# Optimization experiments

Measured on AMD Instinct MI355X. Metric: run time of the kernel, lower is better.

The kernel has to match this reference:

```python
import jax, jax.numpy as jnp
import numpy as np

N, E, F_IN, H, C, ED, NODES = 25000, 100000, 16, 4, 280, 6, 6


def setup_inputs() -> dict:
    key = jax.random.key(0)
    ks = jax.random.split(key, 16)
    s = lambda k, sh: jax.random.normal(k, sh, dtype=jnp.float32) * 0.05
    return {
        "x": jax.random.normal(ks[0], (N, F_IN), dtype=jnp.float32),
        "edge_index": jax.random.randint(ks[1], (2, E), 0, N, dtype=jnp.int64),
        "edge_attr": jax.random.normal(ks[2], (E, ED), dtype=jnp.float32),
        # TransformerConv params (PyG): lin_query/key/value (bias), lin_edge (no bias), lin_skip (bias)
        "Wq": s(ks[3], (F_IN, H * C)), "bq": jnp.zeros((H * C,), jnp.float32),
        "Wk": s(ks[4], (F_IN, H * C)), "bk": jnp.zeros((H * C,), jnp.float32),
        "Wv": s(ks[5], (F_IN, H * C)), "bv": jnp.zeros((H * C,), jnp.float32),
        "We": s(ks[6], (ED, H * C)),
        "Wskip": s(ks[7], (F_IN, C)), "bskip": jnp.zeros((C,), jnp.float32),
        # MLP: 280 -> 64 -> 16 -> NODES, softmax
        "W1": s(ks[8], (280, 64)), "b1": jnp.zeros((64,), jnp.float32),
        "W2": s(ks[9], (64, 16)), "b2": jnp.zeros((16,), jnp.float32),
        "W3": s(ks[10], (16, NODES)), "b3": jnp.zeros((NODES,), jnp.float32),
    }


def reference(x, edge_index, edge_attr, Wq, bq, Wk, bk, Wv, bv, We, Wskip, bskip, W1, b1, W2, b2, W3, b3):
    n = x.shape[0]
    src, dst = edge_index[0], edge_index[1]  # message j -> i (PyG convention)
    q = (x @ Wq + bq).reshape(n, H, C)
    k = (x @ Wk + bk).reshape(n, H, C)
    v = (x @ Wv + bv).reshape(n, H, C)
    e = (edge_attr @ We).reshape(-1, H, C)  # [E,H,C]
    kj = k[src] + e                          # gather + edge features
    alpha = jnp.einsum('ehc,ehc->eh', q[dst], kj) / jnp.sqrt(jnp.float32(C))  # [E,H]
    # numerically stable segment softmax over destination nodes
    amax = jax.ops.segment_max(alpha, dst, num_segments=n)
    ex = jnp.exp(alpha - amax[dst])
    denom = jax.ops.segment_sum(ex, dst, num_segments=n)
    attn = ex / (denom[dst] + 1e-16)
    out = jax.ops.segment_sum(attn[..., None] * (v[src] + e), dst, num_segments=n)  # [N,H,C]
    out = out.mean(axis=1)                  # concat=False -> mean over heads
    out = out + x @ Wskip + bskip           # root/skip connection
    h = out.reshape(-1, 280)
    h = jax.nn.relu(h @ W1 + b1)
    h = jax.nn.relu(h @ W2 + b2)
    return jax.nn.softmax(h @ W3 + b3, axis=-1)
```

## Files before the change

### kernel.cpp

```cpp
#include <hip/hip_runtime.h>

#define N_NODES 25000
#define N_EDGES 100000
#define NPAD 25024
#define CH 280
#define HC 1120
#define CAP 32

typedef unsigned int uint;
typedef unsigned short ushort;
typedef __attribute__((ext_vector_type(8))) short short8;
typedef __attribute__((ext_vector_type(4))) float f32x4;

#define FAC_A 0
#define FAC_B 1024
#define FAC_C 1408
#define FAC_D 1472
#define FAC_F 1536
#define FAC_G 1560
#define FAC_TOTAL 1564

#define WC_K 128

#define PREP_FAC_END   25
#define PREP_WC_END    54
#define PREP_W2_END    55
#define PREP_FILL_END  446
#define PREP_TOTAL     544

__device__ __forceinline__ ushort f2bf(float f) {
  union { float f; uint u; } c; c.f = f;
  uint u = c.u + 0x7FFFu + ((c.u >> 16) & 1u);
  return (ushort)(u >> 16);
}

__global__ __launch_bounds__(256) void prep_kernel(
    const float* __restrict__ Wq, const float* __restrict__ Wk,
    const float* __restrict__ We, const float* __restrict__ bq,
    const float* __restrict__ bk, float* __restrict__ fac,
    const float* __restrict__ Wv, const float* __restrict__ bv,
    const float* __restrict__ Wskip, const float* __restrict__ bskip,
    const float* __restrict__ W1, const float* __restrict__ b1,
    ushort* __restrict__ Wct,
    const float* __restrict__ W2, ushort* __restrict__ W2tg,
    const int* __restrict__ ei, const float* __restrict__ ea,
    int* __restrict__ cursor, float* __restrict__ erec,
    const float* __restrict__ x, ushort* __restrict__ Vb) {
  int b = blockIdx.x;
  if (b < PREP_FAC_END) {
    int t4 = b * 256 + threadIdx.x;
    int q = t4 >> 2, li = t4 & 3;
    if (q >= FAC_TOTAL) return;
    const float *pa, *pb;
    if (q < FAC_B) {
      int h = q >> 8, f = (q >> 4) & 15, g = q & 15;
      pa = Wq + f * HC + h * CH; pb = Wk + g * HC + h * CH;
    } else if (q < FAC_C) {
      int u = q - FAC_B; int h = u / 96, v2 = u % 96, f = v2 / 6, j = v2 % 6;
      pa = Wq + f * HC + h * CH; pb = We + j * HC + h * CH;
    } else if (q < FAC_D) {
      int u = q - FAC_C; int h = u >> 4, f = u & 15;
      pa = Wq + f * HC + h * CH; pb = bk + h * CH;
    } else if (q < FAC_F) {
      int u = q - FAC_D; int h = u >> 4, g = u & 15;
      pa = Wk + g * HC + h * CH; pb = bq + h * CH;
    } else if (q < FAC_G) {
      int u = q - FAC_F; int h = u / 6, j = u % 6;
      pa = We + j * HC + h * CH; pb = bq + h * CH;
    } else {
      int h = q - FAC_G;
      pa = bq + h * CH; pb = bk + h * CH;
    }
    float acc = 0.f;
    int c0 = li * 70;
    for (int c = c0; c < c0 + 70; ++c) acc = fmaf(pa[c], pb[c], acc);
    acc += __shfl_xor(acc, 1);
    acc += __shfl_xor(acc, 2);
    if (li == 0) fac[q] = acc;
  } else if (b < PREP_WC_END) {
    int wid = threadIdx.x >> 6;
    int r = __builtin_amdgcn_readfirstlane((b - PREP_FAC_END) * 4 + wid);
    if (r >= 113) return;
    int k = threadIdx.x & 63;
    const float* w = nullptr;
    float scale = 1.f;
    bool zero = false;
    if (r < 96) {
      int h = r / 24, j = r % 24;
      if (j == 23) zero = true;
      else {
        if (j < 16) w = Wv + j * HC + h * CH;
        else if (j < 22) w = We + (j - 16) * HC + h * CH;
        else w = bv + h * CH;
        scale = 0.25f;
      }
    } else if (r < 112) {
      w = Wskip + (r - 96) * CH;
    } else {
      w = bskip;
    }
    if (zero) return;
    float acc = 0.f;
    for (int c = 0; c < CH; ++c) acc = fmaf(w[c], W1[c * 64 + k], acc);
    float v = acc * scale;
    if (r == 112) v += b1[k];
    Wct[k * WC_K + r] = f2bf(v);
  } else if (b < PREP_W2_END) {
    for (int t = threadIdx.x; t < 1024; t += 256) {
      int m2 = t >> 6, k = t & 63;
      W2tg[m2 * 64 + k] = f2bf(W2[(size_t)k * 16 + m2]);
    }
  } else if (b < PREP_FILL_END) {
    int e = (b - PREP_W2_END) * 256 + threadIdx.x;
    if (e >= N_EDGES) return;
    int src = ei[e];
    int dst = ei[N_EDGES + e];
    int pos = atomicAdd(&cursor[dst], 1);
    if (pos >= CAP) return;
    const float2* s2 = (const float2*)(ea + (size_t)e * 6);
    float2 e01 = s2[0], e23 = s2[1], e45 = s2[2];
    int4 w0;
    w0.x = src;
    w0.y = __float_as_int(e01.x); w0.z = __float_as_int(e01.y);
    w0.w = __float_as_int(e23.x);
    float4 w1 = make_float4(e23.y, e45.x, e45.y, 0.f);
    float* dstp = erec + ((size_t)dst * CAP + pos) * 8;
    *(int4*)dstp = w0;
    *(float4*)(dstp + 4) = w1;
  } else {
    int n = (b - PREP_FILL_END) * 256 + threadIdx.x;
    if (n >= N_NODES) return;
    const float4* x4 = (const float4*)(x + (size_t)n * 16);
    float xv[16];
#pragma unroll
    for (int i = 0; i < 4; ++i) {
      float4 q = x4[i];
      xv[4 * i] = q.x; xv[4 * i + 1] = q.y; xv[4 * i + 2] = q.z; xv[4 * i + 3] = q.w;
    }
    uint pk[8];
#pragma unroll
    for (int i = 0; i < 8; ++i)
      pk[i] = (uint)f2bf(xv[2 * i]) | ((uint)f2bf(xv[2 * i + 1]) << 16);
    int4* vp = (int4*)(Vb + (size_t)n * WC_K + 96);
    int4 s0, s1, s2, s3;
    s0.x = (int)pk[0]; s0.y = (int)pk[1]; s0.z = (int)pk[2]; s0.w = (int)pk[3];
    s1.x = (int)pk[4]; s1.y = (int)pk[5]; s1.z = (int)pk[6]; s1.w = (int)pk[7];
    s2.x = (int)0x3F80u; s2.y = 0; s2.z = 0; s2.w = 0;
    s3.x = 0; s3.y = 0; s3.z = 0; s3.w = 0;
    vp[0] = s0; vp[1] = s1; vp[2] = s2; vp[3] = s3;
  }
}

__global__ __launch_bounds__(256) void attn_kernel(
    const float* __restrict__ x, const float* __restrict__ fac,
    const float* __restrict__ erec, const int* __restrict__ cursor,
    ushort* __restrict__ Vb) {
  const float RS = 0.05976143046671968f;
  int h = blockIdx.y;
  int wid = threadIdx.x >> 6, lane = threadIdx.x & 63;
  int sub = lane >> 2, half = lane & 3;
  int n = (blockIdx.x * 4 + wid) * 16 + sub;
  if (n >= N_NODES) return;
  float xv[16];
  {
    const float4* x4 = (const float4*)(x + (size_t)n * 16);
#pragma unroll
    for (int i = 0; i < 4; ++i) {
      float4 q = x4[i];
      xv[4 * i] = q.x; xv[4 * i + 1] = q.y; xv[4 * i + 2] = q.z; xv[4 * i + 3] = q.w;
    }
  }
  const float* A  = fac + FAC_A + h * 256;
  const float* B  = fac + FAC_B + h * 96;
  const float* cf = fac + FAC_C + h * 16;
  const float* df = fac + FAC_D + h * 16;
  const float* ff = fac + FAC_F + h * 6;
  const float  gf = fac[FAC_G + h];
  float va[16];
#pragma unroll
  for (int g = 0; g < 16; ++g) {
    float a = df[g];
#pragma unroll
    for (int f = 0; f < 16; ++f) a = fmaf(xv[f], A[f * 16 + g], a);
    va[g] = a;
  }
  float ve[6];
#pragma unroll
  for (int j = 0; j < 6; ++j) {
    float a = ff[j];
#pragma unroll
    for (int f = 0; f < 16; ++f) a = fmaf(xv[f], B[f * 6 + j], a);
    ve[j] = a;
  }
  float v22 = gf;
#pragma unroll
  for (int f = 0; f < 16; ++f) v22 = fmaf(xv[f], cf[f], v22);

  int dg = cursor[n];
  if (dg > CAP) dg = CAP;
  float m = -1e30f, den = 0.f;
  float Sx[16];
  float Sa[6];
#pragma unroll
  for (int f = 0; f < 16; ++f) Sx[f] = 0.f;
#pragma unroll
  for (int j = 0; j < 6; ++j) Sa[j] = 0.f;
  for (int q2 = half; q2 < dg; q2 += 4) {
    const float* er = erec + ((size_t)n * CAP + q2) * 8;
    int4 ra = *(const int4*)er;
    float4 rb = *(const float4*)(er + 4);
    int s = ra.x;
    const float4* xs4 = (const float4*)(x + (size_t)s * 16);
    float4 a0 = xs4[0], a1 = xs4[1], a2 = xs4[2], a3 = xs4[3];
    float xs[16] = {a0.x, a0.y, a0.z, a0.w, a1.x, a1.y, a1.z, a1.w,
                    a2.x, a2.y, a2.z, a2.w, a3.x, a3.y, a3.z, a3.w};
    float eav[6] = {__int_as_float(ra.y), __int_as_float(ra.z),
                    __int_as_float(ra.w), rb.x, rb.y, rb.z};
    float alpha = v22;
#pragma unroll
    for (int f = 0; f < 16; ++f) alpha = fmaf(va[f], xs[f], alpha);
#pragma unroll
    for (int j = 0; j < 6; ++j) alpha = fmaf(ve[j], eav[j], alpha);
    alpha *= RS;
    float nm = fmaxf(m, alpha);
    float sc = __expf(m - nm);
    float w = __expf(alpha - nm);
    den = den * sc + w;
#pragma unroll
    for (int f = 0; f < 16; ++f) Sx[f] = fmaf(Sx[f], sc, w * xs[f]);
#pragma unroll
    for (int j = 0; j < 6; ++j) Sa[j] = fmaf(Sa[j], sc, w * eav[j]);
    m = nm;
  }
#pragma unroll
  for (int d = 1; d <= 2; d <<= 1) {
    float mo  = __shfl_xor(m, d);
    float dno = __shfl_xor(den, d);
    float mm = fmaxf(m, mo);
    float sa = __expf(m - mm);
    float sb = __expf(mo - mm);
    den = den * sa + dno * sb;
#pragma unroll
    for (int f = 0; f < 16; ++f) {
      float so = __shfl_xor(Sx[f], d);
      Sx[f] = Sx[f] * sa + so * sb;
    }
#pragma unroll
    for (int j = 0; j < 6; ++j) {
      float so = __shfl_xor(Sa[j], d);
      Sa[j] = Sa[j] * sa + so * sb;
    }
    m = mm;
  }
  if (half) return;
  float inv = 1.f / (den + 1e-16f);
  float outv[24];
#pragma unroll
  for (int f = 0; f < 16; ++f) outv[f] = Sx[f] * inv;
#pragma unroll
  for (int j = 0; j < 6; ++j) outv[16 + j] = Sa[j] * inv;
  outv[22] = den * inv;
  outv[23] = 0.f;
  uint pk[12];
#pragma unroll
  for (int i = 0; i < 12; ++i)
    pk[i] = (uint)f2bf(outv[2 * i]) | ((uint)f2bf(outv[2 * i + 1]) << 16);
  int4* vp = (int4*)(Vb + (size_t)n * WC_K + h * 24);
  int4 s0, s1, s2;
  s0.x = (int)pk[0]; s0.y = (int)pk[1]; s0.z = (int)pk[2]; s0.w = (int)pk[3];
  s1.x = (int)pk[4]; s1.y = (int)pk[5]; s1.z = (int)pk[6]; s1.w = (int)pk[7];
  s2.x = (int)pk[8]; s2.y = (int)pk[9]; s2.z = (int)pk[10]; s2.w = (int)pk[11];
  vp[0] = s0; vp[1] = s1; vp[2] = s2;
}

__global__ __launch_bounds__(256) void mlp_kernel(
    const ushort* __restrict__ Vb, const ushort* __restrict__ Wct,
    const ushort* __restrict__ W2tg, const float* __restrict__ b2,
    const float* __restrict__ W3, const float* __restrict__ b3,
    float* __restrict__ out) {
  __shared__ ushort Wcs[64 * 136];
  __shared__ ushort W2ts[16 * 72];
  __shared__ ushort h1b[64 * 72];
  __shared__ float  h2s[64 * 17];
  int tid = threadIdx.x;
  int wid = tid >> 6, lane = tid & 63;
  int col15 = lane & 15, quad = lane >> 4;
  {
    int row = tid >> 2, seg = tid & 3;
    const ushort* src = Wct + row * 128 + seg * 32;
    ushort* dst = Wcs + row * 136 + seg * 32;
#pragma unroll
    for (int i = 0; i < 4; ++i)
      *(int4*)(dst + i * 8) = *(const int4*)(src + i * 8);
  }
  if (tid < 128) {
    int row = tid >> 3, seg = tid & 7;
    *(int4*)(W2ts + row * 72 + seg * 8) = *(const int4*)(W2tg + row * 64 + seg * 8);
  }
  __syncthreads();
  int node = blockIdx.x * 64 + wid * 16 + col15;
  f32x4 acc[4];
#pragma unroll
  for (int T = 0; T < 4; ++T) acc[T] = (f32x4){0.f, 0.f, 0.f, 0.f};
#pragma unroll
  for (int kk = 0; kk < 4; ++kk) {
    int k0 = kk * 32;
    short8 a = *(const short8*)(Vb + (size_t)node * WC_K + k0 + quad * 8);
#pragma unroll
    for (int T = 0; T < 4; ++T) {
      short8 bfr = *(const short8*)(Wcs + (T * 16 + col15) * 136 + k0 + quad * 8);
      acc[T] = __builtin_amdgcn_mfma_f32_16x16x32_bf16(a, bfr, acc[T], 0, 0, 0);
    }
  }
#pragma unroll
  for (int T = 0; T < 4; ++T) {
#pragma unroll
    for (int r = 0; r < 4; ++r) {
      int nloc = wid * 16 + quad * 4 + r;
      int c = T * 16 + col15;
      h1b[nloc * 72 + c] = f2bf(fmaxf(acc[T][r], 0.f));
    }
  }
  __syncthreads();
  float b2v = b2[col15];
  f32x4 acc2 = (f32x4){0.f, 0.f, 0.f, 0.f};
#pragma unroll
  for (int kk = 0; kk < 2; ++kk) {
    int k0 = kk * 32;
    short8 a2 = *(const short8*)(h1b + (wid * 16 + col15) * 72 + k0 + quad * 8);
    short8 bf2 = *(const short8*)(W2ts + col15 * 72 + k0 + quad * 8);
    acc2 = __builtin_amdgcn_mfma_f32_16x16x32_bf16(a2, bf2, acc2, 0, 0, 0);
  }
#pragma unroll
  for (int r = 0; r < 4; ++r) {
    int nloc = wid * 16 + quad * 4 + r;
    h2s[nloc * 17 + col15] = fmaxf(acc2[r] + b2v, 0.f);
  }
  __syncthreads();
  if (tid < 64) {
    int n = blockIdx.x * 64 + tid;
    if (n < N_NODES) {
      float hv[16];
#pragma unroll
      for (int j = 0; j < 16; ++j) hv[j] = h2s[tid * 17 + j];
      float lg[6];
      float mx = -1e30f;
#pragma unroll
      for (int o = 0; o < 6; ++o) {
        float a = b3[o];
#pragma unroll
        for (int j = 0; j < 16; ++j) a = fmaf(hv[j], W3[j * 6 + o], a);
        lg[o] = a; mx = fmaxf(mx, a);
      }
      float s = 0.f;
#pragma unroll
      for (int o = 0; o < 6; ++o) { lg[o] = __expf(lg[o] - mx); s += lg[o]; }
      float inv = 1.f / s;
      float2* o2 = (float2*)(out + (size_t)n * 6);
      o2[0] = make_float2(lg[0] * inv, lg[1] * inv);
      o2[1] = make_float2(lg[2] * inv, lg[3] * inv);
      o2[2] = make_float2(lg[4] * inv, lg[5] * inv);
    }
  }
}

extern "C" void kernel_launch(void* const* d_in, const int* in_sizes, int n_in,
                              void* d_out, int out_size, void* d_ws, size_t ws_size,
                              hipStream_t stream) {
  const float* x     = (const float*)d_in[0];
  const int*   ei    = (const int*)d_in[1];
  const float* ea    = (const float*)d_in[2];
  const float* Wq    = (const float*)d_in[3];
  const float* bq    = (const float*)d_in[4];
  const float* Wk    = (const float*)d_in[5];
  const float* bk    = (const float*)d_in[6];
  const float* Wv    = (const float*)d_in[7];
  const float* bv    = (const float*)d_in[8];
  const float* We    = (const float*)d_in[9];
  const float* Wskip = (const float*)d_in[10];
  const float* bskip = (const float*)d_in[11];
  const float* W1    = (const float*)d_in[12];
  const float* b1    = (const float*)d_in[13];
  const float* W2    = (const float*)d_in[14];
  const float* b2    = (const float*)d_in[15];
  const float* W3    = (const float*)d_in[16];
  const float* b3    = (const float*)d_in[17];
  float* out = (float*)d_out;
  (void)in_sizes; (void)n_in; (void)out_size; (void)ws_size;

  char* ws = (char*)d_ws;
  size_t off = 0;
  auto alloc = [&](size_t bytes) {
    void* p = ws + off;
    off = (off + bytes + 255) & ~(size_t)255;
    return p;
  };
  float*  fac      = (float*)alloc(FAC_TOTAL * 4);
  ushort* Wct      = (ushort*)alloc(64 * WC_K * 2);
  int*    cursor   = (int*)alloc(N_NODES * 4);
  ushort* W2tg     = (ushort*)alloc(16 * 64 * 2);
  ushort* Vb       = (ushort*)alloc((size_t)NPAD * WC_K * 2);
  float*  erec     = (float*)alloc((size_t)N_NODES * CAP * 8 * 4);

  hipMemsetAsync(Wct, 0, 64 * WC_K * 2 + N_NODES * 4, stream);
  prep_kernel<<<PREP_TOTAL, 256, 0, stream>>>(
      Wq, Wk, We, bq, bk, fac, Wv, bv, Wskip, bskip, W1, b1, Wct, W2, W2tg,
      ei, ea, cursor, erec, x, Vb);
  attn_kernel<<<dim3(391, 4), 256, 0, stream>>>(x, fac, erec, cursor, Vb);
  mlp_kernel<<<391, 256, 0, stream>>>(Vb, Wct, W2tg, b2, W3, b3, out);
}
```

Baseline: 125.9 us.

## Fuse prep, attention and MLP kernels into one cooperative persistent kernel

Replaces the memset plus three separate kernel launches with a single cooperative kernel that uses grid-wide syncs between phases. Blocks loop over the former grid indices, and the cursor zeroing moves inside the kernel. The Wct zero-fill becomes explicit writes instead of a memset. This removes launch and inter-kernel gaps, but adds grid-sync costs and caps the grid at 512 blocks with occupancy 2, which could reduce parallelism for the attention phase.

```diff
diff --git a/kernel.cpp b/kernel.cpp
--- a/kernel.cpp
+++ b/kernel.cpp
@@ -1,4 +1,7 @@
 #include <hip/hip_runtime.h>
+#include <hip/hip_cooperative_groups.h>
+
+namespace cg = cooperative_groups;
 
 #define N_NODES 25000
 #define N_EDGES 100000
@@ -6,6 +9,7 @@
 #define CH 280
 #define HC 1120
 #define CAP 32
+#define MAXGRID 512
 
 typedef unsigned int uint;
 typedef unsigned short ushort;
@@ -22,11 +26,19 @@
 
 #define WC_K 128
 
-#define PREP_FAC_END   25
-#define PREP_WC_END    54
-#define PREP_W2_END    55
-#define PREP_FILL_END  446
-#define PREP_TOTAL     544
+#define S_FAC_END  25
+#define S_WC_END   57
+#define S_W2_END   58
+#define S_FILL_END 449
+#define S_TOTAL    547
+
+struct KArgs {
+  const float *x; const int *ei; const float *ea;
+  const float *Wq, *bq, *Wk, *bk, *Wv, *bv, *We, *Wskip, *bskip;
+  const float *W1, *b1v, *W2, *b2, *W3, *b3;
+  float *out;
+  float *fac; ushort *Wct; int *cursor; ushort *W2tg; ushort *Vb; float *erec;
+};
 
 __device__ __forceinline__ ushort f2bf(float f) {
   union { float f; uint u; } c; c.f = f;
@@ -34,360 +46,344 @@
   return (ushort)(u >> 16);
 }
 
-__global__ __launch_bounds__(256) void prep_kernel(
-    const float* __restrict__ Wq, const float* __restrict__ Wk,
-    const float* __restrict__ We, const float* __restrict__ bq,
-    const float* __restrict__ bk, float* __restrict__ fac,
-    const float* __restrict__ Wv, const float* __restrict__ bv,
-    const float* __restrict__ Wskip, const float* __restrict__ bskip,
-    const float* __restrict__ W1, const float* __restrict__ b1,
-    ushort* __restrict__ Wct,
-    const float* __restrict__ W2, ushort* __restrict__ W2tg,
-    const int* __restrict__ ei, const float* __restrict__ ea,
-    int* __restrict__ cursor, float* __restrict__ erec,
-    const float* __restrict__ x, ushort* __restrict__ Vb) {
-  int b = blockIdx.x;
-  if (b < PREP_FAC_END) {
-    int t4 = b * 256 + threadIdx.x;
-    int q = t4 >> 2, li = t4 & 3;
-    if (q >= FAC_TOTAL) return;
-    const float *pa, *pb;
-    if (q < FAC_B) {
-      int h = q >> 8, f = (q >> 4) & 15, g = q & 15;
-      pa = Wq + f * HC + h * CH; pb = Wk + g * HC + h * CH;
-    } else if (q < FAC_C) {
-      int u = q - FAC_B; int h = u / 96, v2 = u % 96, f = v2 / 6, j = v2 % 6;
-      pa = Wq + f * HC + h * CH; pb = We + j * HC + h * CH;
-    } else if (q < FAC_D) {
-      int u = q - FAC_C; int h = u >> 4, f = u & 15;
-      pa = Wq + f * HC + h * CH; pb = bk + h * CH;
-    } else if (q < FAC_F) {
-      int u = q - FAC_D; int h = u >> 4, g = u & 15;
-      pa = Wk + g * HC + h * CH; pb = bq + h * CH;
-    } else if (q < FAC_G) {
-      int u = q - FAC_F; int h = u / 6, j = u % 6;
-      pa = We + j * HC + h * CH; pb = bq + h * CH;
-    } else {
-      int h = q - FAC_G;
-      pa = bq + h * CH; pb = bk + h * CH;
-    }
-    float acc = 0.f;
-    int c0 = li * 70;
-    for (int c = c0; c < c0 + 70; ++c) acc = fmaf(pa[c], pb[c], acc);
-    acc += __shfl_xor(acc, 1);
-    acc += __shfl_xor(acc, 2);
-    if (li == 0) fac[q] = acc;
-  } else if (b < PREP_WC_END) {
-    int wid = threadIdx.x >> 6;
-    int r = __builtin_amdgcn_readfirstlane((b - PREP_FAC_END) * 4 + wid);
-    if (r >= 113) return;
-    int k = threadIdx.x & 63;
-    const float* w = nullptr;
-    float scale = 1.f;
-    bool zero = false;
-    if (r < 96) {
-      int h = r / 24, j = r % 24;
-      if (j == 23) zero = true;
-      else {
-        if (j < 16) w = Wv + j * HC + h * CH;
-        else if (j < 22) w = We + (j - 16) * HC + h * CH;
-        else w = bv + h * CH;
-        scale = 0.25f;
-      }
-    } else if (r < 112) {
-      w = Wskip + (r - 96) * CH;
-    } else {
-      w = bskip;
-    }
-    if (zero) return;
-    float acc = 0.f;
-    for (int c = 0; c < CH; ++c) acc = fmaf(w[c], W1[c * 64 + k], acc);
-    float v = acc * scale;
-    if (r == 112) v += b1[k];
-    Wct[k * WC_K + r] = f2bf(v);
-  } else if (b < PREP_W2_END) {
-    for (int t = threadIdx.x; t < 1024; t += 256) {
-      int m2 = t >> 6, k = t & 63;
-      W2tg[m2 * 64 + k] = f2bf(W2[(size_t)k * 16 + m2]);
-    }
-  } else if (b < PREP_FILL_END) {
-    int e = (b - PREP_W2_END) * 256 + threadIdx.x;
-    if (e >= N_EDGES) return;
-    int src = ei[e];
-    int dst = ei[N_EDGES + e];
-    int pos = atomicAdd(&cursor[dst], 1);
-    if (pos >= CAP) return;
-    const float2* s2 = (const float2*)(ea + (size_t)e * 6);
-    float2 e01 = s2[0], e23 = s2[1], e45 = s2[2];
-    int4 w0;
-    w0.x = src;
-    w0.y = __float_as_int(e01.x); w0.z = __float_as_int(e01.y);
-    w0.w = __float_as_int(e23.x);
-    float4 w1 = make_float4(e23.y, e45.x, e45.y, 0.f);
-    float* dstp = erec + ((size_t)dst * CAP + pos) * 8;
-    *(int4*)dstp = w0;
-    *(float4*)(dstp + 4) = w1;
-  } else {
-    int n = (b - PREP_FILL_END) * 256 + threadIdx.x;
-    if (n >= N_NODES) return;
-    const float4* x4 = (const float4*)(x + (size_t)n * 16);
-    float xv[16];
-#pragma unroll
-    for (int i = 0; i < 4; ++i) {
-      float4 q = x4[i];
-      xv[4 * i] = q.x; xv[4 * i + 1] = q.y; xv[4 * i + 2] = q.z; xv[4 * i + 3] = q.w;
-    }
-    uint pk[8];
-#pragma unroll
-    for (int i = 0; i < 8; ++i)
-      pk[i] = (uint)f2bf(xv[2 * i]) | ((uint)f2bf(xv[2 * i + 1]) << 16);
-    int4* vp = (int4*)(Vb + (size_t)n * WC_K + 96);
-    int4 s0, s1, s2, s3;
-    s0.x = (int)pk[0]; s0.y = (int)pk[1]; s0.z = (int)pk[2]; s0.w = (int)pk[3];
-    s1.x = (int)pk[4]; s1.y = (int)pk[5]; s1.z = (int)pk[6]; s1.w = (int)pk[7];
-    s2.x = (int)0x3F80u; s2.y = 0; s2.z = 0; s2.w = 0;
-    s3.x = 0; s3.y = 0; s3.z = 0; s3.w = 0;
-    vp[0] = s0; vp[1] = s1; vp[2] = s2; vp[3] = s3;
-  }
-}
-
-__global__ __launch_bounds__(256) void attn_kernel(
-    const float* __restrict__ x, const float* __restrict__ fac,
-    const float* __restrict__ erec, const int* __restrict__ cursor,
-    ushort* __restrict__ Vb) {
-  const float RS = 0.05976143046671968f;
-  int h = blockIdx.y;
-  int wid = threadIdx.x >> 6, lane = threadIdx.x & 63;
-  int sub = lane >> 2, half = lane & 3;
-  int n = (blockIdx.x * 4 + wid) * 16 + sub;
-  if (n >= N_NODES) return;
-  float xv[16];
-  {
-    const float4* x4 = (const float4*)(x + (size_t)n * 16);
-#pragma unroll
-    for (int i = 0; i < 4; ++i) {
-      float4 q = x4[i];
-      xv[4 * i] = q.x; xv[4 * i + 1] = q.y; xv[4 * i + 2] = q.z; xv[4 * i + 3] = q.w;
-    }
-  }
-  const float* A  = fac + FAC_A + h * 256;
-  const float* B  = fac + FAC_B + h * 96;
-  const float* cf = fac + FAC_C + h * 16;
-  const float* df = fac + FAC_D + h * 16;
-  const float* ff = fac + FAC_F + h * 6;
-  const float  gf = fac[FAC_G + h];
-  float va[16];
-#pragma unroll
-  for (int g = 0; g < 16; ++g) {
-    float a = df[g];
-#pragma unroll
-    for (int f = 0; f < 16; ++f) a = fmaf(xv[f], A[f * 16 + g], a);
-    va[g] = a;
-  }
-  float ve[6];
-#pragma unroll
-  for (int j = 0; j < 6; ++j) {
-    float a = ff[j];
-#pragma unroll
-    for (int f = 0; f < 16; ++f) a = fmaf(xv[f], B[f * 6 + j], a);
-    ve[j] = a;
-  }
-  float v22 = gf;
-#pragma unroll
-  for (int f = 0; f < 16; ++f) v22 = fmaf(xv[f], cf[f], v22);
-
-  int dg = cursor[n];
-  if (dg > CAP) dg = CAP;
-  float m = -1e30f, den = 0.f;
-  float Sx[16];
-  float Sa[6];
-#pragma unroll
-  for (int f = 0; f < 16; ++f) Sx[f] = 0.f;
-#pragma unroll
-  for (int j = 0; j < 6; ++j) Sa[j] = 0.f;
-  for (int q2 = half; q2 < dg; q2 += 4) {
-    const float* er = erec + ((size_t)n * CAP + q2) * 8;
-    int4 ra = *(const int4*)er;
-    float4 rb = *(const float4*)(er + 4);
-    int s = ra.x;
-    const float4* xs4 = (const float4*)(x + (size_t)s * 16);
-    float4 a0 = xs4[0], a1 = xs4[1], a2 = xs4[2], a3 = xs4[3];
-    float xs[16] = {a0.x, a0.y, a0.z, a0.w, a1.x, a1.y, a1.z, a1.w,
-                    a2.x, a2.y, a2.z, a2.w, a3.x, a3.y, a3.z, a3.w};
-    float eav[6] = {__int_as_float(ra.y), __int_as_float(ra.z),
-                    __int_as_float(ra.w), rb.x, rb.y, rb.z};
-    float alpha = v22;
-#pragma unroll
-    for (int f = 0; f < 16; ++f) alpha = fmaf(va[f], xs[f], alpha);
-#pragma unroll
-    for (int j = 0; j < 6; ++j) alpha = fmaf(ve[j], eav[j], alpha);
-    alpha *= RS;
-    float nm = fmaxf(m, alpha);
-    float sc = __expf(m - nm);
-    float w = __expf(alpha - nm);
-    den = den * sc + w;
-#pragma unroll
-    for (int f = 0; f < 16; ++f) Sx[f] = fmaf(Sx[f], sc, w * xs[f]);
-#pragma unroll
-    for (int j = 0; j < 6; ++j) Sa[j] = fmaf(Sa[j], sc, w * eav[j]);
-    m = nm;
-  }
-#pragma unroll
-  for (int d = 1; d <= 2; d <<= 1) {
-    float mo  = __shfl_xor(m, d);
-    float dno = __shfl_xor(den, d);
-    float mm = fmaxf(m, mo);
-    float sa = __expf(m - mm);
-    float sb = __expf(mo - mm);
-    den = den * sa + dno * sb;
-#pragma unroll
-    for (int f = 0; f < 16; ++f) {
-      float so = __shfl_xor(Sx[f], d);
-      Sx[f] = Sx[f] * sa + so * sb;
-    }
-#pragma unroll
-    for (int j = 0; j < 6; ++j) {
-      float so = __shfl_xor(Sa[j], d);
-      Sa[j] = Sa[j] * sa + so * sb;
-    }
-    m = mm;
-  }
-  if (half) return;
-  float inv = 1.f / (den + 1e-16f);
-  float outv[24];
-#pragma unroll
-  for (int f = 0; f < 16; ++f) outv[f] = Sx[f] * inv;
-#pragma unroll
-  for (int j = 0; j < 6; ++j) outv[16 + j] = Sa[j] * inv;
-  outv[22] = den * inv;
-  outv[23] = 0.f;
-  uint pk[12];
-#pragma unroll
-  for (int i = 0; i < 12; ++i)
-    pk[i] = (uint)f2bf(outv[2 * i]) | ((uint)f2bf(outv[2 * i + 1]) << 16);
-  int4* vp = (int4*)(Vb + (size_t)n * WC_K + h * 24);
-  int4 s0, s1, s2;
-  s0.x = (int)pk[0]; s0.y = (int)pk[1]; s0.z = (int)pk[2]; s0.w = (int)pk[3];
-  s1.x = (int)pk[4]; s1.y = (int)pk[5]; s1.z = (int)pk[6]; s1.w = (int)pk[7];
-  s2.x = (int)pk[8]; s2.y = (int)pk[9]; s2.z = (int)pk[10]; s2.w = (int)pk[11];
-  vp[0] = s0; vp[1] = s1; vp[2] = s2;
-}
-
-__global__ __launch_bounds__(256) void mlp_kernel(
-    const ushort* __restrict__ Vb, const ushort* __restrict__ Wct,
-    const ushort* __restrict__ W2tg, const float* __restrict__ b2,
-    const float* __restrict__ W3, const float* __restrict__ b3,
-    float* __restrict__ out) {
+__global__ __launch_bounds__(256, 2) void mega_kernel(KArgs A) {
+  cg::grid_group gg = cg::this_grid();
   __shared__ ushort Wcs[64 * 136];
   __shared__ ushort W2ts[16 * 72];
   __shared__ ushort h1b[64 * 72];
   __shared__ float  h2s[64 * 17];
-  int tid = threadIdx.x;
-  int wid = tid >> 6, lane = tid & 63;
-  int col15 = lane & 15, quad = lane >> 4;
-  {
-    int row = tid >> 2, seg = tid & 3;
-    const ushort* src = Wct + row * 128 + seg * 32;
-    ushort* dst = Wcs + row * 136 + seg * 32;
-#pragma unroll
-    for (int i = 0; i < 4; ++i)
-      *(int4*)(dst + i * 8) = *(const int4*)(src + i * 8);
+  const int nblk = gridDim.x;
+  const int tid = threadIdx.x;
+
+  for (int g = blockIdx.x * 256 + tid; g < N_NODES; g += nblk * 256)
+    A.cursor[g] = 0;
+  gg.sync();
+
+  for (int b = blockIdx.x; b < S_TOTAL; b += nblk) {
+    if (b < S_FAC_END) {
+      int t4 = b * 256 + tid;
+      int q = t4 >> 2, li = t4 & 3;
+      if (q < FAC_TOTAL) {
+        const float *pa, *pb;
+        if (q < FAC_B) {
+          int h = q >> 8, f = (q >> 4) & 15, g = q & 15;
+          pa = A.Wq + f * HC + h * CH; pb = A.Wk + g * HC + h * CH;
+        } else if (q < FAC_C) {
+          int u = q - FAC_B; int h = u / 96, v2 = u % 96, f = v2 / 6, j = v2 % 6;
+          pa = A.Wq + f * HC + h * CH; pb = A.We + j * HC + h * CH;
+        } else if (q < FAC_D) {
+          int u = q - FAC_C; int h = u >> 4, f = u & 15;
+          pa = A.Wq + f * HC + h * CH; pb = A.bk + h * CH;
+        } else if (q < FAC_F) {
+          int u = q - FAC_D; int h = u >> 4, g = u & 15;
+          pa = A.Wk + g * HC + h * CH; pb = A.bq + h * CH;
+        } else if (q < FAC_G) {
+          int u = q - FAC_F; int h = u / 6, j = u % 6;
+          pa = A.We + j * HC + h * CH; pb = A.bq + h * CH;
+        } else {
+          int h = q - FAC_G;
+          pa = A.bq + h * CH; pb = A.bk + h * CH;
+        }
+        float acc = 0.f;
+        int c0 = li * 70;
+        for (int c = c0; c < c0 + 70; ++c) acc = fmaf(pa[c], pb[c], acc);
+        acc += __shfl_xor(acc, 1);
+        acc += __shfl_xor(acc, 2);
+        if (li == 0) A.fac[q] = acc;
+      }
+    } else if (b < S_WC_END) {
+      int wid = tid >> 6;
+      int r = __builtin_amdgcn_readfirstlane((b - S_FAC_END) * 4 + wid);
+      int k = tid & 63;
+      float v = 0.f;
+      bool wz = true;
+      if (r < 113) {
+        const float* w = nullptr;
+        float scale = 1.f;
+        bool zero = false;
+        if (r < 96) {
+          int h = r / 24, j = r % 24;
+          if (j == 23) zero = true;
+          else {
+            if (j < 16) w = A.Wv + j * HC + h * CH;
+            else if (j < 22) w = A.We + (j - 16) * HC + h * CH;
+            else w = A.bv + h * CH;
+            scale = 0.25f;
+          }
+        } else if (r < 112) {
+          w = A.Wskip + (r - 96) * CH;
+        } else {
+          w = A.bskip;
+        }
+        if (!zero) {
+          float acc = 0.f;
+          for (int c = 0; c < CH; ++c) acc = fmaf(w[c], A.W1[c * 64 + k], acc);
+          v = acc * scale;
+          if (r == 112) v += A.b1v[k];
+          wz = false;
+        }
+      }
+      A.Wct[k * WC_K + r] = wz ? (ushort)0 : f2bf(v);
+    } else if (b < S_W2_END) {
+      for (int t = tid; t < 1024; t += 256) {
+        int m2 = t >> 6, k = t & 63;
+        A.W2tg[m2 * 64 + k] = f2bf(A.W2[(size_t)k * 16 + m2]);
+      }
+    } else if (b < S_FILL_END) {
+      int e = (b - S_W2_END) * 256 + tid;
+      if (e < N_EDGES) {
+        int src = A.ei[e];
+        int dst = A.ei[N_EDGES + e];
+        int pos = atomicAdd(&A.cursor[dst], 1);
+        if (pos < CAP) {
+          const float2* s2 = (const float2*)(A.ea + (size_t)e * 6);
+          float2 e01 = s2[0], e23 = s2[1], e45 = s2[2];
+          int4 w0;
+          w0.x = src;
+          w0.y = __float_as_int(e01.x); w0.z = __float_as_int(e01.y);
+          w0.w = __float_as_int(e23.x);
+          float4 w1 = make_float4(e23.y, e45.x, e45.y, 0.f);
+          float* dstp = A.erec + ((size_t)dst * CAP + pos) * 8;
+          *(int4*)dstp = w0;
+          *(float4*)(dstp + 4) = w1;
+        }
+      }
+    } else {
+      int n = (b - S_FILL_END) * 256 + tid;
+      if (n < N_NODES) {
+        const float4* x4 = (const float4*)(A.x + (size_t)n * 16);
+        float xv[16];
+#pragma unroll
+        for (int i = 0; i < 4; ++i) {
+          float4 q = x4[i];
+          xv[4 * i] = q.x; xv[4 * i + 1] = q.y; xv[4 * i + 2] = q.z; xv[4 * i + 3] = q.w;
+        }
+        uint pk[8];
+#pragma unroll
+        for (int i = 0; i < 8; ++i)
+          pk[i] = (uint)f2bf(xv[2 * i]) | ((uint)f2bf(xv[2 * i + 1]) << 16);
+        int4* vp = (int4*)(A.Vb + (size_t)n * WC_K + 96);
+        int4 s0, s1, s2, s3;
+        s0.x = (int)pk[0]; s0.y = (int)pk[1]; s0.z = (int)pk[2]; s0.w = (int)pk[3];
+        s1.x = (int)pk[4]; s1.y = (int)pk[5]; s1.z = (int)pk[6]; s1.w = (int)pk[7];
+        s2.x = (int)0x3F80u; s2.y = 0; s2.z = 0; s2.w = 0;
+        s3.x = 0; s3.y = 0; s3.z = 0; s3.w = 0;
+        vp[0] = s0; vp[1] = s1; vp[2] = s2; vp[3] = s3;
+      }
+    }
   }
-  if (tid < 128) {
-    int row = tid >> 3, seg = tid & 7;
-    *(int4*)(W2ts + row * 72 + seg * 8) = *(const int4*)(W2tg + row * 64 + seg * 8);
+  gg.sync();
+
+  const float RS = 0.05976143046671968f;
+  for (int vu = blockIdx.x; vu < 391 * 4; vu += nblk) {
+    int h = vu & 3, bx = vu >> 2;
+    int wid = tid >> 6, lane = tid & 63;
+    int sub = lane >> 2, half = lane & 3;
+    int n = (bx * 4 + wid) * 16 + sub;
+    if (n < N_NODES) {
+      float xv[16];
+      {
+        const float4* x4 = (const float4*)(A.x + (size_t)n * 16);
+#pragma unroll
+        for (int i = 0; i < 4; ++i) {
+          float4 q = x4[i];
+          xv[4 * i] = q.x; xv[4 * i + 1] = q.y; xv[4 * i + 2] = q.z; xv[4 * i + 3] = q.w;
+        }
+      }
+      const float* Af = A.fac + FAC_A + h * 256;
+      const float* Bf = A.fac + FAC_B + h * 96;
+      const float* cf = A.fac + FAC_C + h * 16;
+      const float* df = A.fac + FAC_D + h * 16;
+      const float* ff = A.fac + FAC_F + h * 6;
+      const float  gf = A.fac[FAC_G + h];
+      float va[16];
+#pragma unroll
+      for (int g = 0; g < 16; ++g) {
+        float a = df[g];
+#pragma unroll
+        for (int f = 0; f < 16; ++f) a = fmaf(xv[f], Af[f * 16 + g], a);
+        va[g] = a;
+      }
+      float ve[6];
+#pragma unroll
+      for (int j = 0; j < 6; ++j) {
+        float a = ff[j];
+#pragma unroll
+        for (int f = 0; f < 16; ++f) a = fmaf(xv[f], Bf[f * 6 + j], a);
+        ve[j] = a;
+      }
+      float v22 = gf;
+#pragma unroll
+      for (int f = 0; f < 16; ++f) v22 = fmaf(xv[f], cf[f], v22);
+
+      int dg = A.cursor[n];
+      if (dg > CAP) dg = CAP;
+      float m = -1e30f, den = 0.f;
+      float Sx[16];
+      float Sa[6];
+#pragma unroll
+      for (int f = 0; f < 16; ++f) Sx[f] = 0.f;
+#pragma unroll
+      for (int j = 0; j < 6; ++j) Sa[j] = 0.f;
+      for (int q2 = half; q2 < dg; q2 += 4) {
+        const float* er = A.erec + ((size_t)n * CAP + q2) * 8;
+        int4 ra = *(const int4*)er;
+        float4 rb = *(const float4*)(er + 4);
+        int s = ra.x;
+        const float4* xs4 = (const float4*)(A.x + (size_t)s * 16);
+        float4 a0 = xs4[0], a1 = xs4[1], a2 = xs4[2], a3 = xs4[3];
+        float xs[16] = {a0.x, a0.y, a0.z, a0.w, a1.x, a1.y, a1.z, a1.w,
+                        a2.x, a2.y, a2.z, a2.w, a3.x, a3.y, a3.z, a3.w};
+        float eav[6] = {__int_as_float(ra.y), __int_as_float(ra.z),
+                        __int_as_float(ra.w), rb.x, rb.y, rb.z};
+        float alpha = v22;
+#pragma unroll
+        for (int f = 0; f < 16; ++f) alpha = fmaf(va[f], xs[f], alpha);
+#pragma unroll
+        for (int j = 0; j < 6; ++j) alpha = fmaf(ve[j], eav[j], alpha);
+        alpha *= RS;
+        float nm = fmaxf(m, alpha);
+        float sc = __expf(m - nm);
+        float w = __expf(alpha - nm);
+        den = den * sc + w;
+#pragma unroll
+        for (int f = 0; f < 16; ++f) Sx[f] = fmaf(Sx[f], sc, w * xs[f]);
+#pragma unroll
+        for (int j = 0; j < 6; ++j) Sa[j] = fmaf(Sa[j], sc, w * eav[j]);
+        m = nm;
+      }
+#pragma unroll
+      for (int d = 1; d <= 2; d <<= 1) {
+        float mo  = __shfl_xor(m, d);
+        float dno = __shfl_xor(den, d);
+        float mm = fmaxf(m, mo);
+        float sa = __expf(m - mm);
+        float sb = __expf(mo - mm);
+        den = den * sa + dno * sb;
+#pragma unroll
+        for (int f = 0; f < 16; ++f) {
+          float so = __shfl_xor(Sx[f], d);
+          Sx[f] = Sx[f] * sa + so * sb;
+        }
+#pragma unroll
+        for (int j = 0; j < 6; ++j) {
+          float so = __shfl_xor(Sa[j], d);
+          Sa[j] = Sa[j] * sa + so * sb;
+        }
+        m = mm;
+      }
+      if (half == 0) {
+        float inv = 1.f / (den + 1e-16f);
+        float outv[24];
+#pragma unroll
+        for (int f = 0; f < 16; ++f) outv[f] = Sx[f] * inv;
+#pragma unroll
+        for (int j = 0; j < 6; ++j) outv[16 + j] = Sa[j] * inv;
+        outv[22] = den * inv;
+        outv[23] = 0.f;
+        uint pk[12];
+#pragma unroll
+        for (int i = 0; i < 12; ++i)
+          pk[i] = (uint)f2bf(outv[2 * i]) | ((uint)f2bf(outv[2 * i + 1]) << 16);
+        int4* vp = (int4*)(A.Vb + (size_t)n * WC_K + h * 24);
+        int4 s0, s1, s2;
+        s0.x = (int)pk[0]; s0.y = (int)pk[1]; s0.z = (int)pk[2]; s0.w = (int)pk[3];
+        s1.x = (int)pk[4]; s1.y = (int)pk[5]; s1.z = (int)pk[6]; s1.w = (int)pk[7];
+        s2.x = (int)pk[8]; s2.y = (int)pk[9]; s2.z = (int)pk[10]; s2.w = (int)pk[11];
+        vp[0] = s0; vp[1] = s1; vp[2] = s2;
+      }
+    }
   }
-  __syncthreads();
-  int node = blockIdx.x * 64 + wid * 16 + col15;
-  f32x4 acc[4];
-#pragma unroll
-  for (int T = 0; T < 4; ++T) acc[T] = (f32x4){0.f, 0.f, 0.f, 0.f};
-#pragma unroll
-  for (int kk = 0; kk < 4; ++kk) {
-    int k0 = kk * 32;
-    short8 a = *(const short8*)(Vb + (size_t)node * WC_K + k0 + quad * 8);
+  gg.sync();
+
+  for (int tile = blockIdx.x; tile < 391; tile += nblk) {
+    int wid = tid >> 6, lane = tid & 63;
+    int col15 = lane & 15, quad = lane >> 4;
+    {
+      int row = tid >> 2, seg = tid & 3;
+      const ushort* src = A.Wct + row * 128 + seg * 32;
+      ushort* dst = Wcs + row * 136 + seg * 32;
+#pragma unroll
+      for (int i = 0; i < 4; ++i)
+        *(int4*)(dst + i * 8) = *(const int4*)(src + i * 8);
+    }
+    if (tid < 128) {
+      int row = tid >> 3, seg = tid & 7;
+      *(int4*)(W2ts + row * 72 + seg * 8) = *(const int4*)(A.W2tg + row * 64 + seg * 8);
+    }
+    __syncthreads();
+    int node = tile * 64 + wid * 16 + col15;
+    f32x4 acc[4];
+#pragma unroll
+    for (int T = 0; T < 4; ++T) acc[T] = (f32x4){0.f, 0.f, 0.f, 0.f};
+#pragma unroll
+    for (int kk = 0; kk < 4; ++kk) {
+      int k0 = kk * 32;
+      short8 a = *(const short8*)(A.Vb + (size_t)node * WC_K + k0 + quad * 8);
+#pragma unroll
+      for (int T = 0; T < 4; ++T) {
+        short8 bfr = *(const short8*)(Wcs + (T * 16 + col15) * 136 + k0 + quad * 8);
+        acc[T] = __builtin_amdgcn_mfma_f32_16x16x32_bf16(a, bfr, acc[T], 0, 0, 0);
+      }
+    }
 #pragma unroll
     for (int T = 0; T < 4; ++T) {
-      short8 bfr = *(const short8*)(Wcs + (T * 16 + col15) * 136 + k0 + quad * 8);
-      acc[T] = __builtin_amdgcn_mfma_f32_16x16x32_bf16(a, bfr, acc[T], 0, 0, 0);
-    }
-  }
-#pragma unroll
-  for (int T = 0; T < 4; ++T) {
+#pragma unroll
+      for (int r = 0; r < 4; ++r) {
+        int nloc = wid * 16 + quad * 4 + r;
+        int c = T * 16 + col15;
+        h1b[nloc * 72 + c] = f2bf(fmaxf(acc[T][r], 0.f));
+      }
+    }
+    __syncthreads();
+    float b2v = A.b2[col15];
+    f32x4 acc2 = (f32x4){0.f, 0.f, 0.f, 0.f};
+#pragma unroll
+    for (int kk = 0; kk < 2; ++kk) {
+      int k0 = kk * 32;
+      short8 a2 = *(const short8*)(h1b + (wid * 16 + col15) * 72 + k0 + quad * 8);
+      short8 bf2 = *(const short8*)(W2ts + col15 * 72 + k0 + quad * 8);
+      acc2 = __builtin_amdgcn_mfma_f32_16x16x32_bf16(a2, bf2, acc2, 0, 0, 0);
+    }
 #pragma unroll
     for (int r = 0; r < 4; ++r) {
       int nloc = wid * 16 + quad * 4 + r;
-      int c = T * 16 + col15;
-      h1b[nloc * 72 + c] = f2bf(fmaxf(acc[T][r], 0.f));
-    }
-  }
-  __syncthreads();
-  float b2v = b2[col15];
-  f32x4 acc2 = (f32x4){0.f, 0.f, 0.f, 0.f};
-#pragma unroll
-  for (int kk = 0; kk < 2; ++kk) {
-    int k0 = kk * 32;
-    short8 a2 = *(const short8*)(h1b + (wid * 16 + col15) * 72 + k0 + quad * 8);
-    short8 bf2 = *(const short8*)(W2ts + col15 * 72 + k0 + quad * 8);
-    acc2 = __builtin_amdgcn_mfma_f32_16x16x32_bf16(a2, bf2, acc2, 0, 0, 0);
-  }
-#pragma unroll
-  for (int r = 0; r < 4; ++r) {
-    int nloc = wid * 16 + quad * 4 + r;
-    h2s[nloc * 17 + col15] = fmaxf(acc2[r] + b2v, 0.f);
-  }
-  __syncthreads();
-  if (tid < 64) {
-    int n = blockIdx.x * 64 + tid;
-    if (n < N_NODES) {
-      float hv[16];
-#pragma unroll
-      for (int j = 0; j < 16; ++j) hv[j] = h2s[tid * 17 + j];
-      float lg[6];
-      float mx = -1e30f;
-#pragma unroll
-      for (int o = 0; o < 6; ++o) {
-        float a = b3[o];
-#pragma unroll
-        for (int j = 0; j < 16; ++j) a = fmaf(hv[j], W3[j * 6 + o], a);
-        lg[o] = a; mx = fmaxf(mx, a);
-      }
-      float s = 0.f;
-#pragma unroll
-      for (int o = 0; o < 6; ++o) { lg[o] = __expf(lg[o] - mx); s += lg[o]; }
-      float inv = 1.f / s;
-      float2* o2 = (float2*)(out + (size_t)n * 6);
-      o2[0] = make_float2(lg[0] * inv, lg[1] * inv);
-      o2[1] = make_float2(lg[2] * inv, lg[3] * inv);
-      o2[2] = make_float2(lg[4] * inv, lg[5] * inv);
-    }
+      h2s[nloc * 17 + col15] = fmaxf(acc2[r] + b2v, 0.f);
+    }
+    __syncthreads();
+    if (tid < 64) {
+      int n = tile * 64 + tid;
+      if (n < N_NODES) {
+        float hv[16];
+#pragma unroll
+        for (int j = 0; j < 16; ++j) hv[j] = h2s[tid * 17 + j];
+        float lg[6];
+        float mx = -1e30f;
+#pragma unroll
+        for (int o = 0; o < 6; ++o) {
+          float a = A.b3[o];
+#pragma unroll
+          for (int j = 0; j < 16; ++j) a = fmaf(hv[j], A.W3[j * 6 + o], a);
+          lg[o] = a; mx = fmaxf(mx, a);
+        }
+        float s = 0.f;
+#pragma unroll
+        for (int o = 0; o < 6; ++o) { lg[o] = __expf(lg[o] - mx); s += lg[o]; }
+        float inv = 1.f / s;
+        float2* o2 = (float2*)(A.out + (size_t)n * 6);
+        o2[0] = make_float2(lg[0] * inv, lg[1] * inv);
+        o2[1] = make_float2(lg[2] * inv, lg[3] * inv);
+        o2[2] = make_float2(lg[4] * inv, lg[5] * inv);
+      }
+    }
+    __syncthreads();
   }
 }
 
 extern "C" void kernel_launch(void* const* d_in, const int* in_sizes, int n_in,
                               void* d_out, int out_size, void* d_ws, size_t ws_size,
                               hipStream_t stream) {
-  const float* x     = (const float*)d_in[0];
-  const int*   ei    = (const int*)d_in[1];
-  const float* ea    = (const float*)d_in[2];
-  const float* Wq    = (const float*)d_in[3];
-  const float* bq    = (const float*)d_in[4];
-  const float* Wk    = (const float*)d_in[5];
-  const float* bk    = (const float*)d_in[6];
-  const float* Wv    = (const float*)d_in[7];
-  const float* bv    = (const float*)d_in[8];
-  const float* We    = (const float*)d_in[9];
-  const float* Wskip = (const float*)d_in[10];
-  const float* bskip = (const float*)d_in[11];
-  const float* W1    = (const float*)d_in[12];
-  const float* b1    = (const float*)d_in[13];
-  const float* W2    = (const float*)d_in[14];
-  const float* b2    = (const float*)d_in[15];
-  const float* W3    = (const float*)d_in[16];
-  const float* b3    = (const float*)d_in[17];
-  float* out = (float*)d_out;
   (void)in_sizes; (void)n_in; (void)out_size; (void)ws_size;
-
   char* ws = (char*)d_ws;
   size_t off = 0;
   auto alloc = [&](size_t bytes) {
@@ -395,17 +391,40 @@
     off = (off + bytes + 255) & ~(size_t)255;
     return p;
   };
-  float*  fac      = (float*)alloc(FAC_TOTAL * 4);
-  ushort* Wct      = (ushort*)alloc(64 * WC_K * 2);
-  int*    cursor   = (int*)alloc(N_NODES * 4);
-  ushort* W2tg     = (ushort*)alloc(16 * 64 * 2);
-  ushort* Vb       = (ushort*)alloc((size_t)NPAD * WC_K * 2);
-  float*  erec     = (float*)alloc((size_t)N_NODES * CAP * 8 * 4);
-
-  hipMemsetAsync(Wct, 0, 64 * WC_K * 2 + N_NODES * 4, stream);
-  prep_kernel<<<PREP_TOTAL, 256, 0, stream>>>(
-      Wq, Wk, We, bq, bk, fac, Wv, bv, Wskip, bskip, W1, b1, Wct, W2, W2tg,
-      ei, ea, cursor, erec, x, Vb);
-  attn_kernel<<<dim3(391, 4), 256, 0, stream>>>(x, fac, erec, cursor, Vb);
-  mlp_kernel<<<391, 256, 0, stream>>>(Vb, Wct, W2tg, b2, W3, b3, out);
+  KArgs A;
+  A.x     = (const float*)d_in[0];
+  A.ei    = (const int*)d_in[1];
+  A.ea    = (const float*)d_in[2];
+  A.Wq    = (const float*)d_in[3];
+  A.bq    = (const float*)d_in[4];
+  A.Wk    = (const float*)d_in[5];
+  A.bk    = (const float*)d_in[6];
+  A.Wv    = (const float*)d_in[7];
+  A.bv    = (const float*)d_in[8];
+  A.We    = (const float*)d_in[9];
+  A.Wskip = (const float*)d_in[10];
+  A.bskip = (const float*)d_in[11];
+  A.W1    = (const float*)d_in[12];
+  A.b1v   = (const float*)d_in[13];
+  A.W2    = (const float*)d_in[14];
+  A.b2    = (const float*)d_in[15];
+  A.W3    = (const float*)d_in[16];
+  A.b3    = (const float*)d_in[17];
+  A.out   = (float*)d_out;
+  A.fac    = (float*)alloc(FAC_TOTAL * 4);
+  A.Wct    = (ushort*)alloc(64 * WC_K * 2);
+  A.cursor = (int*)alloc(N_NODES * 4);
+  A.W2tg   = (ushort*)alloc(16 * 64 * 2);
+  A.Vb     = (ushort*)alloc((size_t)NPAD * WC_K * 2);
+  A.erec   = (float*)alloc((size_t)N_NODES * CAP * 8 * 4);
+
+  int maxB = 0;
+  if (hipOccupancyMaxActiveBlocksPerMultiprocessor(&maxB, mega_kernel, 256, 0)
+          != hipSuccess || maxB < 1)
+    maxB = 1;
+  int grid = maxB * 256;
+  if (grid > MAXGRID) grid = MAXGRID;
+  void* kp[] = {(void*)&A};
+  hipLaunchCooperativeKernel((const void*)mega_kernel, dim3(grid), dim3(256),
+                             kp, 0, stream);
 }
```

After: 262.9 us. 109% more time.
